# Kernel optimization log

Hardware: AMD Instinct MI355X
Metric: run time of the kernel (lower is better)

Reference implementation:

```python
import jax, jax.numpy as jnp
import numpy as np

A4 = 0.1
EPS = 1e-8  # torch.cosine_similarity eps


def setup_inputs() -> dict:
    key = jax.random.key(0)
    ks = jax.random.split(key, 7)
    N, D, C = 200000, 256, 7
    return {
        "seq": jax.random.normal(ks[0], (N, D), jnp.float32),
        "seq1": jax.random.normal(ks[1], (N, D), jnp.float32),
        "prompt": jax.random.normal(ks[2], (3, D), jnp.float32),
        "w_np": jnp.array([[0.5, 0.4, 0.3]], jnp.float32),  # weighted_prompt init
        "w_ds": jax.random.normal(ks[4], (1, D), jnp.float32) * 0.05,  # downstreamprompt weight
        "w_df": jnp.array([[0.0, 1.0]], jnp.float32),  # weighted_feature init
        "ave": jax.random.normal(ks[6], (C, D), jnp.float32),  # class prototypes (train=0)
    }


def reference(seq, seq1, prompt, w_np, w_ds, w_df, ave):
    # weighted_prompt -> ELU -> 1 + .
    weight = 1.0 + jax.nn.elu(w_np @ prompt)          # [1, D]
    rawret1 = weight * seq                             # [N, D]
    rawret2 = w_ds * seq                               # downstreamprompt
    rawret3 = jax.nn.elu(w_df[0, 0] * rawret1 + w_df[0, 1] * rawret2)
    rawret = rawret3 + A4 * seq1                       # [N, D]
    # per-row cosine similarity vs each class prototype, then softmax
    dots = rawret @ ave.T                              # [N, C]
    nr = jnp.linalg.norm(rawret, axis=1, keepdims=True)   # [N, 1]
    na = jnp.linalg.norm(ave, axis=1)                     # [C]
    sims = dots / jnp.maximum(nr * na[None, :], EPS)
    return jax.nn.softmax(sims, axis=1)
```

## Files before the change

### kernel.cpp

```cpp
#include <hip/hip_runtime.h>
#include <math.h>


__device__ __forceinline__ float elu1(float x) {
    return x > 0.0f ? x : __expf(x) - 1.0f;
}

__device__ __forceinline__ float wave_sum(float v) {
#pragma unroll
    for (int off = 32; off > 0; off >>= 1)
        v += __shfl_xor(v, off, 64);
    return v;
}

__global__ __launch_bounds__(256) void downprompt_kernel(
    const float* __restrict__ seq,
    const float* __restrict__ seq1,
    const float* __restrict__ prompt,
    const float* __restrict__ w_np,
    const float* __restrict__ w_ds,
    const float* __restrict__ w_df,
    const float* __restrict__ ave,
    float* __restrict__ out,
    int N)
{
    const int lane = threadIdx.x & 63;
    const int wavesPerBlock = blockDim.x >> 6;
    const int gwave = blockIdx.x * wavesPerBlock + (threadIdx.x >> 6);
    const int nwave = gridDim.x * wavesPerBlock;
    const int d0 = lane << 2;

    const float a  = w_df[0];
    const float b  = w_df[1];
    const float w0 = w_np[0], w1 = w_np[1], w2 = w_np[2];

    const float4 p0 = *(const float4*)(prompt +   0 + d0);
    const float4 p1 = *(const float4*)(prompt + 256 + d0);
    const float4 p2 = *(const float4*)(prompt + 512 + d0);
    const float4 wd = *(const float4*)(w_ds + d0);

    float coef[4];
    coef[0] = a * (1.0f + elu1(w0*p0.x + w1*p1.x + w2*p2.x)) + b * wd.x;
    coef[1] = a * (1.0f + elu1(w0*p0.y + w1*p1.y + w2*p2.y)) + b * wd.y;
    coef[2] = a * (1.0f + elu1(w0*p0.z + w1*p1.z + w2*p2.z)) + b * wd.z;
    coef[3] = a * (1.0f + elu1(w0*p0.w + w1*p1.w + w2*p2.w)) + b * wd.w;

    float av[7][4];
    float na[7];
#pragma unroll
    for (int c = 0; c < 7; ++c) {
        const float4 v = *(const float4*)(ave + c * 256 + d0);
        av[c][0] = v.x; av[c][1] = v.y; av[c][2] = v.z; av[c][3] = v.w;
        const float p = v.x*v.x + v.y*v.y + v.z*v.z + v.w*v.w;
        na[c] = sqrtf(wave_sum(p));
    }

    for (int row = gwave; row < N; row += nwave) {
        const float4 s = *(const float4*)(seq  + (size_t)row * 256 + d0);
        const float4 t = *(const float4*)(seq1 + (size_t)row * 256 + d0);

        float r[4];
        r[0] = elu1(coef[0] * s.x) + 0.1f * t.x;
        r[1] = elu1(coef[1] * s.y) + 0.1f * t.y;
        r[2] = elu1(coef[2] * s.z) + 0.1f * t.z;
        r[3] = elu1(coef[3] * s.w) + 0.1f * t.w;

        float acc[8];
#pragma unroll
        for (int c = 0; c < 7; ++c)
            acc[c] = r[0]*av[c][0] + r[1]*av[c][1] + r[2]*av[c][2] + r[3]*av[c][3];
        acc[7] = r[0]*r[0] + r[1]*r[1] + r[2]*r[2] + r[3]*r[3];

#pragma unroll
        for (int off = 32; off > 0; off >>= 1) {
#pragma unroll
            for (int k = 0; k < 8; ++k)
                acc[k] += __shfl_xor(acc[k], off, 64);
        }

        const float nr = sqrtf(acc[7]);
        float sims[7];
        float m = -INFINITY;
#pragma unroll
        for (int c = 0; c < 7; ++c) {
            const float den = fmaxf(nr * na[c], 1e-8f);
            sims[c] = acc[c] * __builtin_amdgcn_rcpf(den);
            m = fmaxf(m, sims[c]);
        }
        float sum = 0.0f, mye = 0.0f;
#pragma unroll
        for (int c = 0; c < 7; ++c) {
            const float e = __expf(sims[c] - m);
            sum += e;
            if (lane == c) mye = e;
        }
        if (lane < 7)
            out[(size_t)row * 7 + lane] = mye * __builtin_amdgcn_rcpf(sum);
    }
}

extern "C" void kernel_launch(void* const* d_in, const int* in_sizes, int n_in,
                              void* d_out, int out_size, void* d_ws, size_t ws_size,
                              hipStream_t stream) {
    const float* seq    = (const float*)d_in[0];
    const float* seq1   = (const float*)d_in[1];
    const float* prompt = (const float*)d_in[2];
    const float* w_np   = (const float*)d_in[3];
    const float* w_ds   = (const float*)d_in[4];
    const float* w_df   = (const float*)d_in[5];
    const float* ave    = (const float*)d_in[6];
    float* out = (float*)d_out;

    const int N = in_sizes[0] / 256;

    downprompt_kernel<<<2048, 256, 0, stream>>>(seq, seq1, prompt, w_np, w_ds,
                                                w_df, ave, out, N);
}
```

Before: 443.3 us.

## Process 16 rows per wave with 4 lanes per row and LDS-staged prototypes

Each wave now handles 16 rows at once, with 4 lanes per row looping over 16 float4 column chunks. The cross-lane reduction shrinks from a 6-step to a 2-step shuffle for all 8 accumulators, and all 64 lanes store output instead of 7. The coefficients and class prototypes move into shared memory, and the grid is sized to give each wave about two row groups. The intent is to cut shuffle and reduction overhead per row and keep more memory loads in flight per lane. The cost is more LDS reads per element and a strided access pattern per row.

```diff
diff --git a/kernel.cpp b/kernel.cpp
--- a/kernel.cpp
+++ b/kernel.cpp
@@ -24,55 +24,72 @@
     float* __restrict__ out,
     int N)
 {
-    const int lane = threadIdx.x & 63;
-    const int wavesPerBlock = blockDim.x >> 6;
-    const int gwave = blockIdx.x * wavesPerBlock + (threadIdx.x >> 6);
-    const int nwave = gridDim.x * wavesPerBlock;
-    const int d0 = lane << 2;
+    __shared__ float s_coef[256];
+    __shared__ float s_ave[7][256];
 
-    const float a  = w_df[0];
-    const float b  = w_df[1];
-    const float w0 = w_np[0], w1 = w_np[1], w2 = w_np[2];
+    const int tid  = threadIdx.x;
+    const int lane = tid & 63;
 
-    const float4 p0 = *(const float4*)(prompt +   0 + d0);
-    const float4 p1 = *(const float4*)(prompt + 256 + d0);
-    const float4 p2 = *(const float4*)(prompt + 512 + d0);
-    const float4 wd = *(const float4*)(w_ds + d0);
+    {
+        const float a  = w_df[0];
+        const float b  = w_df[1];
+        const float w0 = w_np[0], w1 = w_np[1], w2 = w_np[2];
+        const float pr = w0 * prompt[tid] + w1 * prompt[256 + tid]
+                       + w2 * prompt[512 + tid];
+        s_coef[tid] = a * (1.0f + elu1(pr)) + b * w_ds[tid];
+#pragma unroll
+        for (int c = 0; c < 7; ++c)
+            s_ave[c][tid] = ave[c * 256 + tid];
+    }
+    __syncthreads();
 
-    float coef[4];
-    coef[0] = a * (1.0f + elu1(w0*p0.x + w1*p1.x + w2*p2.x)) + b * wd.x;
-    coef[1] = a * (1.0f + elu1(w0*p0.y + w1*p1.y + w2*p2.y)) + b * wd.y;
-    coef[2] = a * (1.0f + elu1(w0*p0.z + w1*p1.z + w2*p2.z)) + b * wd.z;
-    coef[3] = a * (1.0f + elu1(w0*p0.w + w1*p1.w + w2*p2.w)) + b * wd.w;
-
-    float av[7][4];
     float na[7];
 #pragma unroll
     for (int c = 0; c < 7; ++c) {
-        const float4 v = *(const float4*)(ave + c * 256 + d0);
-        av[c][0] = v.x; av[c][1] = v.y; av[c][2] = v.z; av[c][3] = v.w;
-        const float p = v.x*v.x + v.y*v.y + v.z*v.z + v.w*v.w;
-        na[c] = sqrtf(wave_sum(p));
+        const float4 v = *(const float4*)&s_ave[c][lane << 2];
+        na[c] = sqrtf(wave_sum(v.x * v.x + v.y * v.y + v.z * v.z + v.w * v.w));
     }
 
-    for (int row = gwave; row < N; row += nwave) {
-        const float4 s = *(const float4*)(seq  + (size_t)row * 256 + d0);
-        const float4 t = *(const float4*)(seq1 + (size_t)row * 256 + d0);
+    const int q   = lane & 3;
+    const int sub = lane >> 2;
+    const int wavesPerBlock = blockDim.x >> 6;
+    const int gwave = blockIdx.x * wavesPerBlock + (tid >> 6);
+    const int nwave = gridDim.x * wavesPerBlock;
+    const int ngroups = (N + 15) >> 4;
 
-        float r[4];
-        r[0] = elu1(coef[0] * s.x) + 0.1f * t.x;
-        r[1] = elu1(coef[1] * s.y) + 0.1f * t.y;
-        r[2] = elu1(coef[2] * s.z) + 0.1f * t.z;
-        r[3] = elu1(coef[3] * s.w) + 0.1f * t.w;
+    for (int g = gwave; g < ngroups; g += nwave) {
+        const int row = (g << 4) + sub;
+        if (row >= N) continue;
+
+        const float* ps = seq  + (size_t)row * 256;
+        const float* pt = seq1 + (size_t)row * 256;
 
         float acc[8];
 #pragma unroll
-        for (int c = 0; c < 7; ++c)
-            acc[c] = r[0]*av[c][0] + r[1]*av[c][1] + r[2]*av[c][2] + r[3]*av[c][3];
-        acc[7] = r[0]*r[0] + r[1]*r[1] + r[2]*r[2] + r[3]*r[3];
+        for (int k = 0; k < 8; ++k) acc[k] = 0.0f;
+
+#pragma unroll 4
+        for (int i = 0; i < 16; ++i) {
+            const int col = (i << 4) + (q << 2);
+            const float4 s  = *(const float4*)(ps + col);
+            const float4 t  = *(const float4*)(pt + col);
+            const float4 cf = *(const float4*)&s_coef[col];
+
+            const float r0 = elu1(cf.x * s.x) + 0.1f * t.x;
+            const float r1 = elu1(cf.y * s.y) + 0.1f * t.y;
+            const float r2 = elu1(cf.z * s.z) + 0.1f * t.z;
+            const float r3 = elu1(cf.w * s.w) + 0.1f * t.w;
+
+            acc[7] += r0 * r0 + r1 * r1 + r2 * r2 + r3 * r3;
+#pragma unroll
+            for (int c = 0; c < 7; ++c) {
+                const float4 av = *(const float4*)&s_ave[c][col];
+                acc[c] += r0 * av.x + r1 * av.y + r2 * av.z + r3 * av.w;
+            }
+        }
 
 #pragma unroll
-        for (int off = 32; off > 0; off >>= 1) {
+        for (int off = 1; off <= 2; off <<= 1) {
 #pragma unroll
             for (int k = 0; k < 8; ++k)
                 acc[k] += __shfl_xor(acc[k], off, 64);
@@ -87,15 +104,21 @@
             sims[c] = acc[c] * __builtin_amdgcn_rcpf(den);
             m = fmaxf(m, sims[c]);
         }
-        float sum = 0.0f, mye = 0.0f;
+        float e[7], sum = 0.0f;
 #pragma unroll
         for (int c = 0; c < 7; ++c) {
-            const float e = __expf(sims[c] - m);
-            sum += e;
-            if (lane == c) mye = e;
+            e[c] = __expf(sims[c] - m);
+            sum += e[c];
         }
-        if (lane < 7)
-            out[(size_t)row * 7 + lane] = mye * __builtin_amdgcn_rcpf(sum);
+        const float inv = __builtin_amdgcn_rcpf(sum);
+
+        const float eq  = (q == 0) ? e[0] : (q == 1) ? e[1]
+                        : (q == 2) ? e[2] : e[3];
+        const float eq4 = (q == 0) ? e[4] : (q == 1) ? e[5] : e[6];
+
+        float* po = out + (size_t)row * 7;
+        po[q] = eq * inv;
+        if (q < 3) po[q + 4] = eq4 * inv;
     }
 }
 
@@ -112,7 +135,11 @@
     float* out = (float*)d_out;
 
     const int N = in_sizes[0] / 256;
+    const int ngroups = (N + 15) / 16;
+    const int wavesPerBlock = 4;
+    int blocks = (ngroups + wavesPerBlock * 2 - 1) / (wavesPerBlock * 2);
+    if (blocks < 1) blocks = 1;
 
-    downprompt_kernel<<<2048, 256, 0, stream>>>(seq, seq1, prompt, w_np, w_ds,
-                                                w_df, ave, out, N);
+    downprompt_kernel<<<blocks, 256, 0, stream>>>(seq, seq1, prompt, w_np, w_ds,
+                                                  w_df, ave, out, N);
 }
```

Result: faster. 431.7 us (-2.6%).
